# Performance work log

Hardware: AMD Instinct MI355X
Metric: run time of the kernel (lower is better)

## Reference

```python
import jax, jax.numpy as jnp
import numpy as np

B, T, HIN = 4, 2048, 1024
H, E = 16, 64


def setup_inputs() -> dict:
    key = jax.random.key(0)
    k1, k2, k3, k4, k5 = jax.random.split(key, 5)
    s = 1.0 / np.sqrt(HIN)
    return {
        "query": jax.random.normal(k1, (B, T, HIN), dtype=jnp.float32),
        "key_value": jax.random.normal(k2, (B, T, HIN), dtype=jnp.float32),
        "Wq": jax.random.uniform(k3, (HIN, H * E), dtype=jnp.float32, minval=-s, maxval=s),
        "Wk": jax.random.uniform(k4, (HIN, H * E), dtype=jnp.float32, minval=-s, maxval=s),
        "Wv": jax.random.uniform(k5, (HIN, H * E), dtype=jnp.float32, minval=-s, maxval=s),
    }


def reference(query, key_value, Wq, Wk, Wv):
    b, t, _ = query.shape
    scale = E ** (-0.25)  # applied to both q and k, matching e**(1/4) division
    q = (query @ Wq).reshape(b, t, H, E) * scale      # [b,t,h,e]
    k = (key_value @ Wk).reshape(b, t, H, E) * scale  # [b,t,h,e]
    v = (key_value @ Wv).reshape(b, t, H, E)          # [b,t,h,e]
    dot = jnp.einsum("bqhe,bkhe->bhqk", q, k)         # [b,h,t,t]
    attn = jax.nn.softmax(dot, axis=-1)
    out = jnp.einsum("bhqk,bkhe->bqhe", attn, v)      # [b,t,h,e]
    return out.reshape(b, t, H * E)
```

## Files before the change

### kernel.cpp

```cpp
#include <hip/hip_runtime.h>
#include <hip/hip_bf16.h>
#include <stdint.h>


typedef __bf16 bf16;
typedef __attribute__((ext_vector_type(8))) __bf16 bf16x8;
typedef __attribute__((ext_vector_type(4))) float f32x4;
typedef __attribute__((ext_vector_type(16))) float f32x16;
typedef __attribute__((ext_vector_type(4))) unsigned int u32x4;
typedef __attribute__((ext_vector_type(2))) unsigned int u32x2;

#define B_    4
#define T_    2048
#define HIN_  1024
#define H_    16
#define E_    64
#define NOUT_ 1024
#define LOG2E 1.4426950408889634f
#define QKSCALE 0.35355339059327373f
#define QSCALE  (QKSCALE * LOG2E)

__device__ __forceinline__ void gl_lds16(const void* g, void* l) {
  __builtin_amdgcn_global_load_lds((__attribute__((address_space(1))) void*)g,
                                   (__attribute__((address_space(3))) void*)l,
                                   16, 0, 0);
}

__global__ __launch_bounds__(256) void cvt_kernel(const float* __restrict__ Xq,
                                                  const float* __restrict__ Xkv,
                                                  bf16* __restrict__ Xb) {
  const float* src = blockIdx.y ? Xkv : Xq;
  bf16* dst = Xb + (size_t)blockIdx.y * (8192 * 1024);
  size_t i = ((size_t)blockIdx.x * 256 + threadIdx.x) * 8;
  float4 f0 = ((const float4*)(src + i))[0];
  float4 f1 = ((const float4*)(src + i))[1];
  bf16x8 t = {(bf16)f0.x, (bf16)f0.y, (bf16)f0.z, (bf16)f0.w,
              (bf16)f1.x, (bf16)f1.y, (bf16)f1.z, (bf16)f1.w};
  *(bf16x8*)(dst + i) = t;
}

__global__ __launch_bounds__(256) void wt_kernel(const float* __restrict__ Wq,
                                                 const float* __restrict__ Wk,
                                                 const float* __restrict__ Wv,
                                                 bf16* __restrict__ Wt) {
  __shared__ float s[32][33];
  const int z = blockIdx.z;
  const float* W = (z == 0) ? Wq : ((z == 1) ? Wk : Wv);
  bf16* out = Wt + (size_t)z * HIN_ * NOUT_;
  const int n0 = blockIdx.x * 32, k0 = blockIdx.y * 32;
  const int tx = threadIdx.x, ty = threadIdx.y;
#pragma unroll
  for (int i = 0; i < 4; i++)
    s[ty + i * 8][tx] = W[(size_t)(k0 + ty + i * 8) * NOUT_ + n0 + tx];
  __syncthreads();
#pragma unroll
  for (int i = 0; i < 4; i++)
    out[(size_t)(n0 + ty + i * 8) * HIN_ + k0 + tx] = (bf16)s[tx][ty + i * 8];
}

__global__ __launch_bounds__(256, 4) void proj_kernel(const bf16* __restrict__ Xb,
                                                      const bf16* __restrict__ Wt,
                                                      bf16* __restrict__ Qb,
                                                      bf16* __restrict__ Kb,
                                                      bf16* __restrict__ Vtb) {
  __shared__ bf16 As[128 * 64];
  __shared__ bf16 Bs[128 * 64];
  const int z = blockIdx.z;
  const bf16* Abase = (z == 0) ? Xb : ((z == 1) ? Xb + (size_t)8192 * 1024 : Wt + (size_t)2 * HIN_ * NOUT_);
  const bf16* Bbase = (z == 0) ? Wt : ((z == 1) ? Wt + (size_t)HIN_ * NOUT_ : Xb + (size_t)8192 * 1024);
  const int mt = (z == 2) ? blockIdx.y : blockIdx.x;
  const int nt = (z == 2) ? blockIdx.x : blockIdx.y;
  const int m0 = mt * 128, n0 = nt * 128;
  const int tid = threadIdx.x;
  const int w = tid >> 6, lane = tid & 63, quad = lane >> 4, lo = lane & 15;
  const int wm = (w >> 1) * 64, wn = (w & 1) * 64;
  const int srow = w * 8 + (lane >> 3);
  const int schunk = (lane & 7) ^ (srow & 7);

  f32x4 acc[4][4] = {};

  for (int k0 = 0; k0 < HIN_; k0 += 64) {
    __syncthreads();
#pragma unroll
    for (int j = 0; j < 4; j++) {
      int row = j * 32 + srow;
      gl_lds16(Abase + (size_t)(m0 + row) * HIN_ + k0 + schunk * 8, As + (j * 32 + w * 8) * 64);
      gl_lds16(Bbase + (size_t)(n0 + row) * HIN_ + k0 + schunk * 8, Bs + (j * 32 + w * 8) * 64);
    }
    __syncthreads();
#pragma unroll
    for (int kk = 0; kk < 2; kk++) {
      bf16x8 bfrag[4], afrag[4];
#pragma unroll
      for (int j = 0; j < 4; j++) {
        int off = ((((kk << 2) + quad) ^ (lo & 7)) << 3);
        bfrag[j] = *(const bf16x8*)(Bs + (wn + j * 16 + lo) * 64 + off);
        afrag[j] = *(const bf16x8*)(As + (wm + j * 16 + lo) * 64 + off);
      }
#pragma unroll
      for (int i = 0; i < 4; i++)
#pragma unroll
        for (int j = 0; j < 4; j++)
          acc[i][j] = __builtin_amdgcn_mfma_f32_16x16x32_bf16(afrag[i], bfrag[j], acc[i][j], 0, 0, 0);
    }
  }

#pragma unroll
  for (int i = 0; i < 4; i++)
#pragma unroll
    for (int j = 0; j < 4; j++)
#pragma unroll
      for (int r = 0; r < 4; r++) {
        int m = m0 + wm + i * 16 + quad * 4 + r;
        int n = n0 + wn + j * 16 + lo;
        float v = acc[i][j][r];
        if (z == 2) {
          int h = m >> 6, e = m & 63, b = n >> 11, t = n & 2047;
          Vtb[(((size_t)b * H_ + h) * E_ + e) * T_ + t] = (bf16)v;
        } else {
          int b = m >> 11, t = m & 2047, h = n >> 6, e = n & 63;
          if (z == 0)
            Qb[(((size_t)b * H_ + h) * T_ + t) * E_ + e] = (bf16)(v * QSCALE);
          else
            Kb[(((size_t)b * H_ + h) * T_ + t) * E_ + e] = (bf16)(v * QKSCALE);
        }
      }
}

__global__ __launch_bounds__(64, 2) void attn_kernel(const bf16* __restrict__ Qb,
                                                     const bf16* __restrict__ Kb,
                                                     const bf16* __restrict__ Vtb,
                                                     float* __restrict__ out) {
  __shared__ bf16 Ks[64 * 64];
  __shared__ bf16 Vts[64 * 64];
  const int lane = threadIdx.x & 63;
  const int l31 = lane & 31, hi = lane >> 5;
  const int bh = blockIdx.x, q0 = blockIdx.y * 64;
  const bf16* Qg = Qb + (size_t)bh * T_ * E_;
  const bf16* Kg = Kb + (size_t)bh * T_ * E_;
  const bf16* Vg = Vtb + (size_t)bh * E_ * T_;
  const int srow = lane >> 3;
  const int schunk = (lane & 7) ^ (srow & 7);

  bf16x8 qf[2][4];
#pragma unroll
  for (int qb = 0; qb < 2; qb++)
#pragma unroll
    for (int ks = 0; ks < 4; ks++)
      qf[qb][ks] = *(const bf16x8*)(Qg + (size_t)(q0 + qb * 32 + l31) * E_ + ks * 16 + hi * 8);

  f32x16 acc[2][2] = {};
  float lsum[2] = {0.f, 0.f};

#pragma unroll
  for (int i = 0; i < 8; i++) {
    int row = i * 8 + srow;
    gl_lds16(Kg + (size_t)row * E_ + schunk * 8, Ks + (i * 8) * 64);
    gl_lds16(Vg + (size_t)row * T_ + schunk * 8, Vts + (i * 8) * 64);
  }

  for (int kt = 0; kt < T_ / 64; kt++) {
    asm volatile("s_waitcnt vmcnt(0)" ::: "memory");
    __builtin_amdgcn_sched_barrier(0);

    bf16x8 kf[2][4];
#pragma unroll
    for (int tb = 0; tb < 2; tb++)
#pragma unroll
      for (int ks = 0; ks < 4; ks++)
        kf[tb][ks] = *(const bf16x8*)(Ks + (tb * 32 + l31) * 64 +
                                      (((2 * ks + hi) ^ (l31 & 7)) << 3));
    bf16x8 vf[4][2];
#pragma unroll
    for (int tc = 0; tc < 4; tc++)
#pragma unroll
      for (int eb = 0; eb < 2; eb++)
        vf[tc][eb] = *(const bf16x8*)(Vts + (eb * 32 + l31) * 64 +
                                      (((2 * tc + hi) ^ (l31 & 7)) << 3));
    asm volatile("s_waitcnt lgkmcnt(0)" ::: "memory");
    __builtin_amdgcn_sched_barrier(0);

    if (kt + 1 < T_ / 64) {
#pragma unroll
      for (int i = 0; i < 8; i++) {
        int row = i * 8 + srow;
        gl_lds16(Kg + (size_t)((kt + 1) * 64 + row) * E_ + schunk * 8, Ks + (i * 8) * 64);
        gl_lds16(Vg + (size_t)row * T_ + (kt + 1) * 64 + schunk * 8, Vts + (i * 8) * 64);
      }
    }

    bf16x8 pf[2][4];
#pragma unroll
    for (int qb = 0; qb < 2; qb++) {
#pragma unroll
      for (int tb = 0; tb < 2; tb++) {
        f32x16 st = {};
#pragma unroll
        for (int ks = 0; ks < 4; ks++)
          st = __builtin_amdgcn_mfma_f32_32x32x16_bf16(kf[tb][ks], qf[qb][ks], st, 0, 0, 0);
        float ex[16];
        float ls = 0.f;
#pragma unroll
        for (int r = 0; r < 16; r++) {
          ex[r] = __builtin_amdgcn_exp2f(st[r]);
          ls += ex[r];
        }
        lsum[qb] += ls;
        unsigned int u[4][2];
#pragma unroll
        for (int g = 0; g < 4; g++)
#pragma unroll
          for (int p = 0; p < 2; p++)
            asm("v_cvt_pk_bf16_f32 %0, %1, %2"
                : "=v"(u[g][p]) : "v"(ex[4 * g + 2 * p]), "v"(ex[4 * g + 2 * p + 1]));
#pragma unroll
        for (int c2 = 0; c2 < 2; c2++) {
          u32x2 s0 = __builtin_amdgcn_permlane32_swap(u[2 * c2][0], u[2 * c2 + 1][0], false, false);
          u32x2 s1 = __builtin_amdgcn_permlane32_swap(u[2 * c2][1], u[2 * c2 + 1][1], false, false);
          u32x4 wv = {s0[0], s1[0], s0[1], s1[1]};
          pf[qb][tb * 2 + c2] = __builtin_bit_cast(bf16x8, wv);
        }
      }
    }

#pragma unroll
    for (int tc = 0; tc < 4; tc++)
#pragma unroll
      for (int eb = 0; eb < 2; eb++)
#pragma unroll
        for (int qb = 0; qb < 2; qb++)
          acc[qb][eb] = __builtin_amdgcn_mfma_f32_32x32x16_bf16(pf[qb][tc], vf[tc][eb], acc[qb][eb], 0, 0, 0);
  }

#pragma unroll
  for (int qb = 0; qb < 2; qb++)
    lsum[qb] += __shfl_xor(lsum[qb], 32);

  const int b = bh >> 4, h = bh & 15;
#pragma unroll
  for (int qb = 0; qb < 2; qb++)
#pragma unroll
    for (int r = 0; r < 16; r++) {
      int qrow = (r & 3) + 8 * (r >> 2) + 4 * hi;
      float linv = __builtin_amdgcn_rcpf(__shfl(lsum[qb], qrow));
      size_t t = q0 + qb * 32 + qrow;
#pragma unroll
      for (int eb = 0; eb < 2; eb++)
        out[((size_t)b * T_ + t) * NOUT_ + h * E_ + eb * 32 + l31] = acc[qb][eb][r] * linv;
    }
}

extern "C" void kernel_launch(void* const* d_in, const int* in_sizes, int n_in,
                              void* d_out, int out_size, void* d_ws, size_t ws_size,
                              hipStream_t stream) {
  const float* Xq  = (const float*)d_in[0];
  const float* Xkv = (const float*)d_in[1];
  const float* Wq  = (const float*)d_in[2];
  const float* Wk  = (const float*)d_in[3];
  const float* Wv  = (const float*)d_in[4];
  float* out = (float*)d_out;

  char* ws = (char*)d_ws;
  bf16* Qb  = (bf16*)(ws);
  bf16* Kb  = (bf16*)(ws + ((size_t)16 << 20));
  bf16* Vtb = (bf16*)(ws + ((size_t)32 << 20));
  bf16* Wt  = (bf16*)(ws + ((size_t)48 << 20));
  bf16* Xb  = (bf16*)d_out;

  hipLaunchKernelGGL(cvt_kernel, dim3(4096, 2), dim3(256), 0, stream, Xq, Xkv, Xb);
  hipLaunchKernelGGL(wt_kernel, dim3(32, 32, 3), dim3(32, 8), 0, stream, Wq, Wk, Wv, Wt);
  hipLaunchKernelGGL(proj_kernel, dim3(64, 8, 3), dim3(256), 0, stream, Xb, Wt, Qb, Kb, Vtb);
  hipLaunchKernelGGL(attn_kernel, dim3(64, 32), dim3(64), 0, stream, Qb, Kb, Vtb, out);
}
```

Baseline: 251.0 us.

## Double-buffer LDS tiles in projection GEMM to overlap loads with MFMA

The projection kernel now keeps two LDS buffers per operand and issues the global-to-LDS loads for the next K tile before computing on the current one, halving the number of barriers per K step. This is meant to hide global load latency behind the MFMA work. LDS use doubles to 64KB per block and launch bounds drop from 4 to 2 blocks per CU, which lowers occupancy.

```diff
diff --git a/kernel.cpp b/kernel.cpp
--- a/kernel.cpp
+++ b/kernel.cpp
@@ -58,13 +58,43 @@
     out[(size_t)(n0 + ty + i * 8) * HIN_ + k0 + tx] = (bf16)s[tx][ty + i * 8];
 }
 
-__global__ __launch_bounds__(256, 4) void proj_kernel(const bf16* __restrict__ Xb,
+#define PROJ_STAGE(BUF, K0V)                                                    \
+  _Pragma("unroll")                                                             \
+  for (int j = 0; j < 4; j++) {                                                 \
+    int row = j * 32 + srow;                                                    \
+    gl_lds16(Abase + (size_t)(m0 + row) * HIN_ + (K0V) + schunk * 8,            \
+             As##BUF + (j * 32 + w * 8) * 64);                                  \
+    gl_lds16(Bbase + (size_t)(n0 + row) * HIN_ + (K0V) + schunk * 8,            \
+             Bs##BUF + (j * 32 + w * 8) * 64);                                  \
+  }
+
+#define PROJ_COMP(BUF)                                                          \
+  _Pragma("unroll")                                                             \
+  for (int kk = 0; kk < 2; kk++) {                                              \
+    bf16x8 bfrag[4], afrag[4];                                                  \
+    _Pragma("unroll")                                                           \
+    for (int j = 0; j < 4; j++) {                                               \
+      int off = ((((kk << 2) + quad) ^ (lo & 7)) << 3);                         \
+      bfrag[j] = *(const bf16x8*)(Bs##BUF + (wn + j * 16 + lo) * 64 + off);     \
+      afrag[j] = *(const bf16x8*)(As##BUF + (wm + j * 16 + lo) * 64 + off);     \
+    }                                                                           \
+    _Pragma("unroll")                                                           \
+    for (int i = 0; i < 4; i++)                                                 \
+      _Pragma("unroll")                                                         \
+      for (int j = 0; j < 4; j++)                                               \
+        acc[i][j] = __builtin_amdgcn_mfma_f32_16x16x32_bf16(afrag[i], bfrag[j], \
+                                                            acc[i][j], 0, 0, 0);\
+  }
+
+__global__ __launch_bounds__(256, 2) void proj_kernel(const bf16* __restrict__ Xb,
                                                       const bf16* __restrict__ Wt,
                                                       bf16* __restrict__ Qb,
                                                       bf16* __restrict__ Kb,
                                                       bf16* __restrict__ Vtb) {
-  __shared__ bf16 As[128 * 64];
-  __shared__ bf16 Bs[128 * 64];
+  __shared__ bf16 As0[128 * 64];
+  __shared__ bf16 As1[128 * 64];
+  __shared__ bf16 Bs0[128 * 64];
+  __shared__ bf16 Bs1[128 * 64];
   const int z = blockIdx.z;
   const bf16* Abase = (z == 0) ? Xb : ((z == 1) ? Xb + (size_t)8192 * 1024 : Wt + (size_t)2 * HIN_ * NOUT_);
   const bf16* Bbase = (z == 0) ? Wt : ((z == 1) ? Wt + (size_t)HIN_ * NOUT_ : Xb + (size_t)8192 * 1024);
@@ -79,30 +109,15 @@
 
   f32x4 acc[4][4] = {};
 
-  for (int k0 = 0; k0 < HIN_; k0 += 64) {
+  PROJ_STAGE(0, 0);
+  __syncthreads();
+  for (int k0 = 0; k0 < HIN_; k0 += 128) {
+    PROJ_STAGE(1, k0 + 64);
+    PROJ_COMP(0);
     __syncthreads();
-#pragma unroll
-    for (int j = 0; j < 4; j++) {
-      int row = j * 32 + srow;
-      gl_lds16(Abase + (size_t)(m0 + row) * HIN_ + k0 + schunk * 8, As + (j * 32 + w * 8) * 64);
-      gl_lds16(Bbase + (size_t)(n0 + row) * HIN_ + k0 + schunk * 8, Bs + (j * 32 + w * 8) * 64);
-    }
+    if (k0 + 128 < HIN_) { PROJ_STAGE(0, k0 + 128); }
+    PROJ_COMP(1);
     __syncthreads();
-#pragma unroll
-    for (int kk = 0; kk < 2; kk++) {
-      bf16x8 bfrag[4], afrag[4];
-#pragma unroll
-      for (int j = 0; j < 4; j++) {
-        int off = ((((kk << 2) + quad) ^ (lo & 7)) << 3);
-        bfrag[j] = *(const bf16x8*)(Bs + (wn + j * 16 + lo) * 64 + off);
-        afrag[j] = *(const bf16x8*)(As + (wm + j * 16 + lo) * 64 + off);
-      }
-#pragma unroll
-      for (int i = 0; i < 4; i++)
-#pragma unroll
-        for (int j = 0; j < 4; j++)
-          acc[i][j] = __builtin_amdgcn_mfma_f32_16x16x32_bf16(afrag[i], bfrag[j], acc[i][j], 0, 0, 0);
-    }
   }
 
 #pragma unroll
```

New measurement: 254.9 us. No clear change (+1.5%).
